# Kernel optimization log

Hardware: AMD Instinct MI355X
Metric: run time of the kernel (lower is better)

The kernel has to match this reference:

```python
import jax, jax.numpy as jnp
import numpy as np

B, S, FEAT, HID, H = 8, 1024, 1024, 1024, 8
DH = HID // H  # head dim = 128
MASK_VAL = -128.0  # mask_val = -2**7 (soft additive mask, per original code)


def setup_inputs() -> dict:
    key = jax.random.key(0)
    ks = jax.random.split(key, 4)
    scale = 0.02
    return {
        "queries": jax.random.normal(ks[0], (B, S, FEAT), dtype=jnp.float32),
        "Wq": jax.random.normal(ks[1], (FEAT, HID), dtype=jnp.float32) * scale,
        "bq": jnp.zeros((HID,), dtype=jnp.float32),
        "Wk": jax.random.normal(ks[2], (FEAT, HID), dtype=jnp.float32) * scale,
        "bk": jnp.zeros((HID,), dtype=jnp.float32),
        "Wv": jax.random.normal(ks[3], (FEAT, HID), dtype=jnp.float32) * scale,
        "bv": jnp.zeros((HID,), dtype=jnp.float32),
    }


def reference(queries, Wq, bq, Wk, bk, Wv, bv):
    # Self-attention: keys = values = queries (torch forward defaults)
    q = queries @ Wq + bq  # [B,S,HID]
    k = queries @ Wk + bk
    v = queries @ Wv + bv
    # split heads: chunk along last dim == reshape (B,S,H,DH)
    qh = q.reshape(B, S, H, DH)
    kh = k.reshape(B, S, H, DH)
    vh = v.reshape(B, S, H, DH)
    # exp-scaled-dot score (non-standard: exp BEFORE mask/softmax)
    logits = jnp.einsum("bqhd,bkhd->bhqk", qh, kh) / np.float32(np.sqrt(DH))
    score = jnp.exp(logits)
    # soft additive causal mask: upper triangle (diag=1) gets -128
    mask = jnp.triu(jnp.full((S, S), MASK_VAL, dtype=score.dtype), k=1)
    att = jax.nn.softmax(score + mask, axis=-1)  # [B,H,S,S]
    ctx = jnp.einsum("bhqk,bkhd->bqhd", att, vh)  # [B,S,H,DH]
    # reverse heads: concat along last dim
    return ctx.reshape(B, S, HID)
```

## Files before the change

### kernel.cpp

```cpp
#include <hip/hip_runtime.h>


typedef __bf16 bf16x8 __attribute__((ext_vector_type(8)));
typedef float floatx4 __attribute__((ext_vector_type(4)));
typedef unsigned short u16;
typedef unsigned int u32;

#define RSCALE 0.08838834764831845f

__device__ __forceinline__ u16 f2b(float f) {
  union { float f; unsigned u; } v; v.f = f;
  return (u16)((v.u + 0x7FFFu + ((v.u >> 16) & 1u)) >> 16);
}

__device__ __forceinline__ void gld_lds16(const void* g, void* l) {
  __builtin_amdgcn_global_load_lds(
      (const __attribute__((address_space(1))) unsigned*)g,
      (__attribute__((address_space(3))) unsigned*)l, 16, 0, 0);
}

#define MFMA16(a, b, c) __builtin_amdgcn_mfma_f32_16x16x32_bf16(a, b, c, 0, 0, 0)

__global__ __launch_bounds__(256) void prep_kernel(
    const float4* __restrict__ X, u16* __restrict__ Xb,
    const float* __restrict__ Wq, const float* __restrict__ Wk,
    const float* __restrict__ Wv, u16* __restrict__ Wtb) {
  if (blockIdx.x < 8192) {
    unsigned i = blockIdx.x * 256u + threadIdx.x;
    float4 v = X[i];
    ushort4 o;
    o.x = f2b(v.x); o.y = f2b(v.y); o.z = f2b(v.z); o.w = f2b(v.w);
    *reinterpret_cast<ushort4*>(Xb + 4u * i) = o;
  } else {
    const int bid = blockIdx.x - 8192;
    const int mat = bid >> 10;
    const int bx = bid & 31, by = (bid >> 5) & 31;
    const float* W = (mat == 0) ? Wq : (mat == 1) ? Wk : Wv;
    u16* Wt = Wtb + (size_t)mat * (1024u * 1024u);
    __shared__ u16 tile[32][33];
    const int x = threadIdx.x & 31, y = threadIdx.x >> 5;
    const int kt = bx * 32, nt = by * 32;
#pragma unroll
    for (int i = 0; i < 4; ++i)
      tile[y + 8 * i][x] = f2b(W[(size_t)(kt + y + 8 * i) * 1024 + nt + x]);
    __syncthreads();
#pragma unroll
    for (int i = 0; i < 4; ++i)
      Wt[(size_t)(nt + y + 8 * i) * 1024 + kt + x] = tile[x][y + 8 * i];
  }
}

__global__ __launch_bounds__(256, 2) void gemm_qkv_kernel(
    const u16* __restrict__ Xb, const u16* __restrict__ Wtb,
    const float* __restrict__ bq, const float* __restrict__ bk,
    const float* __restrict__ bv, u16* __restrict__ Qh, u16* __restrict__ Kh,
    u16* __restrict__ Vt) {
  const int mat = blockIdx.z;
  const u16* __restrict__ Wt = Wtb + (size_t)mat * (1024u * 1024u);
  const float* __restrict__ bias = (mat == 0) ? bq : (mat == 1) ? bk : bv;

  const int m0 = blockIdx.x * 128;
  const int n0 = blockIdx.y * 128;

  __shared__ u16 As[2][128 * 64];
  __shared__ u16 Bs[2][128 * 64];

  const int tid = threadIdx.x;
  const int wid = tid >> 6;
  const int lane = tid & 63;
  const int quad = lane >> 4;
  const int l16 = lane & 15;
  const int wm = (wid & 1) * 64;
  const int wn = (wid >> 1) * 64;

  const floatx4 z4 = {0.f, 0.f, 0.f, 0.f};
  floatx4 acc[4][4];
#pragma unroll
  for (int i = 0; i < 4; ++i)
#pragma unroll
    for (int j = 0; j < 4; ++j) acc[i][j] = z4;

  const int srow = wid * 32;
  const int lrow = lane >> 3;
  const int gblk = (lane & 7) ^ lrow;

  auto stage = [&](int b, int k0) {
#pragma unroll
    for (int c = 0; c < 4; ++c) {
      const int row = srow + c * 8 + lrow;
      gld_lds16(Xb + (size_t)(m0 + row) * 1024 + k0 + gblk * 8,
                As[b] + (srow + c * 8) * 64);
      gld_lds16(Wt + (size_t)(n0 + row) * 1024 + k0 + gblk * 8,
                Bs[b] + (srow + c * 8) * 64);
    }
  };

  stage(0, 0);

  for (int i = 0; i < 16; ++i) {
    __syncthreads();
    if (i < 15) stage((i + 1) & 1, (i + 1) * 64);

    const u16* __restrict__ Ab = As[i & 1];
    const u16* __restrict__ Bb = Bs[i & 1];
#pragma unroll
    for (int c = 0; c < 2; ++c) {
      const int phys = ((c * 4 + quad) ^ (l16 & 7)) * 8;
      bf16x8 af[4], bfr[4];
#pragma unroll
      for (int ii = 0; ii < 4; ++ii)
        af[ii] = *(const bf16x8*)(Ab + (wm + ii * 16 + l16) * 64 + phys);
#pragma unroll
      for (int j = 0; j < 4; ++j)
        bfr[j] = *(const bf16x8*)(Bb + (wn + j * 16 + l16) * 64 + phys);
#pragma unroll
      for (int ii = 0; ii < 4; ++ii)
#pragma unroll
        for (int j = 0; j < 4; ++j)
          acc[ii][j] = MFMA16(af[ii], bfr[j], acc[ii][j]);
    }
  }

  const int b = m0 >> 10;
  const int h = n0 >> 7;
  const int sbase = (m0 & 1023) + wm;
  float bv4[4];
#pragma unroll
  for (int j = 0; j < 4; ++j) bv4[j] = bias[n0 + wn + j * 16 + l16];

  if (mat < 2) {
    u16* outp = (mat == 0 ? Qh : Kh) + (size_t)(b * 8 + h) * 1024 * 128;
#pragma unroll
    for (int i = 0; i < 4; ++i)
#pragma unroll
      for (int j = 0; j < 4; ++j) {
        const int d = wn + j * 16 + l16;
#pragma unroll
        for (int r = 0; r < 4; ++r) {
          const int s = sbase + i * 16 + quad * 4 + r;
          outp[(size_t)s * 128 + d] = f2b(acc[i][j][r] + bv4[j]);
        }
      }
  } else {
    u16* outp = Vt + (size_t)(b * 8 + h) * 128 * 1024;
#pragma unroll
    for (int i = 0; i < 4; ++i)
#pragma unroll
      for (int j = 0; j < 4; ++j) {
        const int d = wn + j * 16 + l16;
        const int s = sbase + i * 16 + quad * 4;
        ushort4 pk;
        pk.x = f2b(acc[i][j][0] + bv4[j]);
        pk.y = f2b(acc[i][j][1] + bv4[j]);
        pk.z = f2b(acc[i][j][2] + bv4[j]);
        pk.w = f2b(acc[i][j][3] + bv4[j]);
        *(ushort4*)(outp + (size_t)d * 1024 + s) = pk;
      }
  }
}

__global__ __launch_bounds__(256, 2) void attn_kernel(const u16* __restrict__ Qh,
                                                      const u16* __restrict__ Kh,
                                                      const u16* __restrict__ Vt,
                                                      float* __restrict__ out) {
  const int id = blockIdx.x;
  const int x = id & 7;
  const int j = id >> 3;
  const int bh = x * 8 + (j & 7);
  const int QTMAP[8] = {7, 5, 6, 4, 0, 2, 1, 3};
  const int qt = QTMAP[j >> 3];
  const int q0 = qt * 128;

  const int tid = threadIdx.x;
  const int wid = tid >> 6;
  const int lane = tid & 63;
  const int quad = lane >> 4;
  const int l16 = lane & 15;

  __shared__ u16 Ks[2][64 * 128];
  __shared__ u16 Vs[2][128 * 64];
  __shared__ u16 Ps[4][32 * 32];

  const u16* __restrict__ Qbase = Qh + (size_t)bh * 1024 * 128;
  const u16* __restrict__ Kbase = Kh + (size_t)bh * 1024 * 128;
  const u16* __restrict__ Vbase = Vt + (size_t)bh * 128 * 1024;

  const int qw = q0 + wid * 32;

  bf16x8 qf[2][4];
#pragma unroll
  for (int nt = 0; nt < 2; ++nt)
#pragma unroll
    for (int c = 0; c < 4; ++c)
      qf[nt][c] = *(const bf16x8*)(Qbase + (size_t)(qw + nt * 16 + l16) * 128 +
                                   c * 32 + quad * 8);

  const floatx4 z4 = {0.f, 0.f, 0.f, 0.f};
  floatx4 o[2][8];
#pragma unroll
  for (int nt = 0; nt < 2; ++nt)
#pragma unroll
    for (int dt = 0; dt < 8; ++dt) o[nt][dt] = z4;
  float lacc[2] = {0.f, 0.f};

  auto stage = [&](int b, int k0) {
#pragma unroll
    for (int c = 0; c < 4; ++c) {
      const int r0 = wid * 16 + c * 4;
      const int row = r0 + quad;
      gld_lds16(Kbase + (size_t)(k0 + row) * 128 + ((l16 ^ (c * 4 + quad)) * 8),
                Ks[b] + r0 * 128);
    }
#pragma unroll
    for (int c = 0; c < 4; ++c) {
      const int r0 = wid * 32 + c * 8;
      const int row = r0 + (lane >> 3);
      gld_lds16(Vbase + (size_t)row * 1024 + k0 +
                    (((lane & 7) ^ ((lane >> 3) & 7)) * 8),
                Vs[b] + r0 * 64);
    }
  };

  const int n = (q0 + 128) >> 6;
  stage(0, 0);

  for (int i = 0; i < n; ++i) {
    const int k0 = i << 6;
    __syncthreads();
    if (i + 1 < n) stage((i + 1) & 1, k0 + 64);

    const u16* __restrict__ Kb = Ks[i & 1];
    const u16* __restrict__ Vb = Vs[i & 1];

#pragma unroll
    for (int half = 0; half < 2; ++half) {
      if (k0 + half * 32 > qw + 31) break;

#pragma unroll
      for (int f2 = 0; f2 < 2; ++f2) {
        const int f = half * 2 + f2;
        bf16x8 kf[4];
#pragma unroll
        for (int c = 0; c < 4; ++c)
          kf[c] = *(const bf16x8*)(Kb + (f * 16 + l16) * 128 +
                                   (((c * 4 + quad) ^ l16) * 8));
        floatx4 st[2];
#pragma unroll
        for (int nt = 0; nt < 2; ++nt) {
          st[nt] = z4;
#pragma unroll
          for (int c = 0; c < 4; ++c) st[nt] = MFMA16(kf[c], qf[nt][c], st[nt]);
        }
        const int kb = k0 + f * 16 + quad * 4;
#pragma unroll
        for (int nt = 0; nt < 2; ++nt) {
          const int qrow = qw + nt * 16 + l16;
          float p[4];
#pragma unroll
          for (int r = 0; r < 4; ++r) {
            const float e = fminf(__expf(st[nt][r] * RSCALE), 85.f);
            p[r] = (kb + r > qrow) ? 0.f : __expf(e);
          }
          lacc[nt] += (p[0] + p[1]) + (p[2] + p[3]);
          uint2 pk;
          pk.x = (u32)f2b(p[0]) | ((u32)f2b(p[1]) << 16);
          pk.y = (u32)f2b(p[2]) | ((u32)f2b(p[3]) << 16);
          *(uint2*)((char*)Ps[wid] + (nt * 16 + l16) * 64 +
                    (((f2 * 2 + (quad >> 1)) ^ (l16 & 3)) * 16) +
                    (quad & 1) * 8) = pk;
        }
      }
      asm volatile("s_waitcnt lgkmcnt(0)" ::: "memory");

      bf16x8 pa[2];
#pragma unroll
      for (int nt = 0; nt < 2; ++nt)
        pa[nt] = *(const bf16x8*)((char*)Ps[wid] + (nt * 16 + l16) * 64 +
                                  ((quad ^ (l16 & 3)) * 16));
#pragma unroll
      for (int dt = 0; dt < 8; ++dt) {
        const bf16x8 vf = *(const bf16x8*)(
            Vb + (dt * 16 + l16) * 64 +
            (((half * 4 + quad) ^ (l16 & 7)) * 8));
        o[0][dt] = MFMA16(vf, pa[0], o[0][dt]);
        o[1][dt] = MFMA16(vf, pa[1], o[1][dt]);
      }
    }
  }

  float linv[2];
#pragma unroll
  for (int nt = 0; nt < 2; ++nt) {
    float s = lacc[nt];
    s += __shfl_xor(s, 16);
    s += __shfl_xor(s, 32);
    linv[nt] = 1.0f / s;
  }

  float* outp = out + (size_t)(bh >> 3) * 1024 * 1024 + (bh & 7) * 128;
#pragma unroll
  for (int nt = 0; nt < 2; ++nt) {
    const int qrow = qw + nt * 16 + l16;
#pragma unroll
    for (int dt = 0; dt < 8; ++dt) {
      float4 v;
      v.x = o[nt][dt][0] * linv[nt];
      v.y = o[nt][dt][1] * linv[nt];
      v.z = o[nt][dt][2] * linv[nt];
      v.w = o[nt][dt][3] * linv[nt];
      *(float4*)(outp + (size_t)qrow * 1024 + dt * 16 + quad * 4) = v;
    }
  }
}

extern "C" void kernel_launch(void* const* d_in, const int* in_sizes, int n_in,
                              void* d_out, int out_size, void* d_ws,
                              size_t ws_size, hipStream_t stream) {
  const float* X = (const float*)d_in[0];
  const float* Wq = (const float*)d_in[1];
  const float* bq = (const float*)d_in[2];
  const float* Wk = (const float*)d_in[3];
  const float* bk = (const float*)d_in[4];
  const float* Wv = (const float*)d_in[5];
  const float* bv = (const float*)d_in[6];
  float* out = (float*)d_out;

  char* ws = (char*)d_ws;
  u16* Xb  = (u16*)(ws);
  u16* Wtb = (u16*)(ws + (16u << 20));
  u16* Qh  = (u16*)(ws + (22u << 20));
  u16* Kh  = (u16*)(ws + (38u << 20));
  u16* Vt  = (u16*)(ws + (54u << 20));

  prep_kernel<<<8192 + 3072, 256, 0, stream>>>((const float4*)X, Xb, Wq, Wk,
                                               Wv, Wtb);
  dim3 gg(64, 8, 3);
  gemm_qkv_kernel<<<gg, 256, 0, stream>>>(Xb, Wtb, bq, bk, bv, Qh, Kh, Vt);
  attn_kernel<<<512, 256, 0, stream>>>(Qh, Kh, Vt, out);
}
```

Baseline: 198.7 us.

## Split prep and QKV GEMM into separate launches, shrink attention key tile to 32

```diff
diff --git a/kernel.cpp b/kernel.cpp
--- a/kernel.cpp
+++ b/kernel.cpp
@@ -21,43 +21,37 @@
 
 #define MFMA16(a, b, c) __builtin_amdgcn_mfma_f32_16x16x32_bf16(a, b, c, 0, 0, 0)
 
-__global__ __launch_bounds__(256) void prep_kernel(
-    const float4* __restrict__ X, u16* __restrict__ Xb,
+__global__ __launch_bounds__(256) void cast_kernel(const float4* __restrict__ X,
+                                                   u16* __restrict__ Xb) {
+  unsigned i = blockIdx.x * 256u + threadIdx.x;
+  float4 v = X[i];
+  ushort4 o;
+  o.x = f2b(v.x); o.y = f2b(v.y); o.z = f2b(v.z); o.w = f2b(v.w);
+  *reinterpret_cast<ushort4*>(Xb + 4u * i) = o;
+}
+
+__global__ __launch_bounds__(256) void transpose_kernel(
     const float* __restrict__ Wq, const float* __restrict__ Wk,
     const float* __restrict__ Wv, u16* __restrict__ Wtb) {
-  if (blockIdx.x < 8192) {
-    unsigned i = blockIdx.x * 256u + threadIdx.x;
-    float4 v = X[i];
-    ushort4 o;
-    o.x = f2b(v.x); o.y = f2b(v.y); o.z = f2b(v.z); o.w = f2b(v.w);
-    *reinterpret_cast<ushort4*>(Xb + 4u * i) = o;
-  } else {
-    const int bid = blockIdx.x - 8192;
-    const int mat = bid >> 10;
-    const int bx = bid & 31, by = (bid >> 5) & 31;
-    const float* W = (mat == 0) ? Wq : (mat == 1) ? Wk : Wv;
-    u16* Wt = Wtb + (size_t)mat * (1024u * 1024u);
-    __shared__ u16 tile[32][33];
-    const int x = threadIdx.x & 31, y = threadIdx.x >> 5;
-    const int kt = bx * 32, nt = by * 32;
-#pragma unroll
-    for (int i = 0; i < 4; ++i)
-      tile[y + 8 * i][x] = f2b(W[(size_t)(kt + y + 8 * i) * 1024 + nt + x]);
-    __syncthreads();
-#pragma unroll
-    for (int i = 0; i < 4; ++i)
-      Wt[(size_t)(nt + y + 8 * i) * 1024 + kt + x] = tile[x][y + 8 * i];
-  }
+  const float* W = (blockIdx.z == 0) ? Wq : (blockIdx.z == 1) ? Wk : Wv;
+  u16* Wt = Wtb + (size_t)blockIdx.z * (1024u * 1024u);
+  __shared__ u16 tile[32][33];
+  const int x = threadIdx.x, y = threadIdx.y;
+  const int kt = blockIdx.x * 32, nt = blockIdx.y * 32;
+#pragma unroll
+  for (int i = 0; i < 4; ++i)
+    tile[y + 8 * i][x] = f2b(W[(size_t)(kt + y + 8 * i) * 1024 + nt + x]);
+  __syncthreads();
+#pragma unroll
+  for (int i = 0; i < 4; ++i)
+    Wt[(size_t)(nt + y + 8 * i) * 1024 + kt + x] = tile[x][y + 8 * i];
 }
 
 __global__ __launch_bounds__(256, 2) void gemm_qkv_kernel(
     const u16* __restrict__ Xb, const u16* __restrict__ Wtb,
-    const float* __restrict__ bq, const float* __restrict__ bk,
-    const float* __restrict__ bv, u16* __restrict__ Qh, u16* __restrict__ Kh,
-    u16* __restrict__ Vt) {
-  const int mat = blockIdx.z;
+    const float* __restrict__ bias, u16* __restrict__ outQK,
+    u16* __restrict__ outVt, const int mat) {
   const u16* __restrict__ Wt = Wtb + (size_t)mat * (1024u * 1024u);
-  const float* __restrict__ bias = (mat == 0) ? bq : (mat == 1) ? bk : bv;
 
   const int m0 = blockIdx.x * 128;
   const int n0 = blockIdx.y * 128;
@@ -129,7 +123,7 @@
   for (int j = 0; j < 4; ++j) bv4[j] = bias[n0 + wn + j * 16 + l16];
 
   if (mat < 2) {
-    u16* outp = (mat == 0 ? Qh : Kh) + (size_t)(b * 8 + h) * 1024 * 128;
+    u16* outp = outQK + (size_t)(b * 8 + h) * 1024 * 128;
 #pragma unroll
     for (int i = 0; i < 4; ++i)
 #pragma unroll
@@ -142,7 +136,7 @@
         }
       }
   } else {
-    u16* outp = Vt + (size_t)(b * 8 + h) * 128 * 1024;
+    u16* outp = outVt + (size_t)(b * 8 + h) * 128 * 1024;
 #pragma unroll
     for (int i = 0; i < 4; ++i)
 #pragma unroll
@@ -164,11 +158,9 @@
                                                       const u16* __restrict__ Vt,
                                                       float* __restrict__ out) {
   const int id = blockIdx.x;
-  const int x = id & 7;
-  const int j = id >> 3;
-  const int bh = x * 8 + (j & 7);
-  const int QTMAP[8] = {7, 5, 6, 4, 0, 2, 1, 3};
-  const int qt = QTMAP[j >> 3];
+  const int bh = (id & 7) * 8 + ((id >> 3) & 7);
+  const int QTMAP[8] = {7, 4, 6, 5, 0, 3, 1, 2};
+  const int qt = QTMAP[id >> 6];
   const int q0 = qt * 128;
 
   const int tid = threadIdx.x;
@@ -177,9 +169,9 @@
   const int quad = lane >> 4;
   const int l16 = lane & 15;
 
-  __shared__ u16 Ks[2][64 * 128];
-  __shared__ u16 Vs[2][128 * 64];
-  __shared__ u16 Ps[4][32 * 32];
+  __shared__ u16 Ks[2][32 * 128];
+  __shared__ u16 Vs[2][64 * 64];
+  __shared__ u16 Ps[4][16 * 64];
 
   const u16* __restrict__ Qbase = Qh + (size_t)bh * 1024 * 128;
   const u16* __restrict__ Kbase = Kh + (size_t)bh * 1024 * 128;
@@ -203,42 +195,41 @@
     for (int dt = 0; dt < 8; ++dt) o[nt][dt] = z4;
   float lacc[2] = {0.f, 0.f};
 
+  const int slr = lane >> 3;
+  const int sp = lane & 7;
+  const int ssub = sp >> 2;
+
   auto stage = [&](int b, int k0) {
 #pragma unroll
-    for (int c = 0; c < 4; ++c) {
-      const int r0 = wid * 16 + c * 4;
+    for (int c = 0; c < 2; ++c) {
+      const int r0 = wid * 8 + c * 4;
       const int row = r0 + quad;
-      gld_lds16(Kbase + (size_t)(k0 + row) * 128 + ((l16 ^ (c * 4 + quad)) * 8),
+      gld_lds16(Kbase + (size_t)(k0 + row) * 128 + ((l16 ^ (row & 15)) * 8),
                 Ks[b] + r0 * 128);
     }
 #pragma unroll
-    for (int c = 0; c < 4; ++c) {
-      const int r0 = wid * 32 + c * 8;
-      const int row = r0 + (lane >> 3);
-      gld_lds16(Vbase + (size_t)row * 1024 + k0 +
-                    (((lane & 7) ^ ((lane >> 3) & 7)) * 8),
-                Vs[b] + r0 * 64);
+    for (int c = 0; c < 2; ++c) {
+      const int r = wid * 16 + c * 8 + slr;
+      const int jj = (sp & 3) ^ (r & 3);
+      gld_lds16(Vbase + (size_t)(2 * r + ssub) * 1024 + k0 + jj * 8,
+                Vs[b] + (wid * 16 + c * 8) * 64);
     }
   };
 
-  const int n = (q0 + 128) >> 6;
+  const int n = (q0 + 128) >> 5;
   stage(0, 0);
 
   for (int i = 0; i < n; ++i) {
-    const int k0 = i << 6;
+    const int k0 = i << 5;
     __syncthreads();
-    if (i + 1 < n) stage((i + 1) & 1, k0 + 64);
-
-    const u16* __restrict__ Kb = Ks[i & 1];
-    const u16* __restrict__ Vb = Vs[i & 1];
-
-#pragma unroll
-    for (int half = 0; half < 2; ++half) {
-      if (k0 + half * 32 > qw + 31) break;
-
-#pragma unroll
-      for (int f2 = 0; f2 < 2; ++f2) {
-        const int f = half * 2 + f2;
+    if (i + 1 < n) stage((i + 1) & 1, k0 + 32);
+
+    if (k0 <= qw + 31) {
+      const u16* __restrict__ Kb = Ks[i & 1];
+      const u16* __restrict__ Vb = Vs[i & 1];
+
+#pragma unroll
+      for (int f = 0; f < 2; ++f) {
         bf16x8 kf[4];
 #pragma unroll
         for (int c = 0; c < 4; ++c)
@@ -265,23 +256,27 @@
           uint2 pk;
           pk.x = (u32)f2b(p[0]) | ((u32)f2b(p[1]) << 16);
           pk.y = (u32)f2b(p[2]) | ((u32)f2b(p[3]) << 16);
-          *(uint2*)((char*)Ps[wid] + (nt * 16 + l16) * 64 +
-                    (((f2 * 2 + (quad >> 1)) ^ (l16 & 3)) * 16) +
-                    (quad & 1) * 8) = pk;
+          const int prow = nt * 8 + (l16 >> 1);
+          const int s8 = f * 4 + quad;
+          *(uint2*)((char*)Ps[wid] + prow * 128 + (l16 & 1) * 64 +
+                    (((s8 >> 1) ^ (prow & 3)) * 16) + (s8 & 1) * 8) = pk;
         }
       }
       asm volatile("s_waitcnt lgkmcnt(0)" ::: "memory");
 
       bf16x8 pa[2];
 #pragma unroll
-      for (int nt = 0; nt < 2; ++nt)
-        pa[nt] = *(const bf16x8*)((char*)Ps[wid] + (nt * 16 + l16) * 64 +
-                                  ((quad ^ (l16 & 3)) * 16));
+      for (int nt = 0; nt < 2; ++nt) {
+        const int prow = nt * 8 + (l16 >> 1);
+        pa[nt] = *(const bf16x8*)((char*)Ps[wid] + prow * 128 +
+                                  (l16 & 1) * 64 + ((quad ^ (prow & 3)) * 16));
+      }
 #pragma unroll
       for (int dt = 0; dt < 8; ++dt) {
-        const bf16x8 vf = *(const bf16x8*)(
-            Vb + (dt * 16 + l16) * 64 +
-            (((half * 4 + quad) ^ (l16 & 7)) * 8));
+        const int d = dt * 16 + l16;
+        const int vr = d >> 1;
+        const bf16x8 vf = *(const bf16x8*)(Vb + vr * 64 + (d & 1) * 32 +
+                                           ((quad ^ (vr & 3)) * 8));
         o[0][dt] = MFMA16(vf, pa[0], o[0][dt]);
         o[1][dt] = MFMA16(vf, pa[1], o[1][dt]);
       }
@@ -332,9 +327,12 @@
   u16* Kh  = (u16*)(ws + (38u << 20));
   u16* Vt  = (u16*)(ws + (54u << 20));
 
-  prep_kernel<<<8192 + 3072, 256, 0, stream>>>((const float4*)X, Xb, Wq, Wk,
-                                               Wv, Wtb);
-  dim3 gg(64, 8, 3);
-  gemm_qkv_kernel<<<gg, 256, 0, stream>>>(Xb, Wtb, bq, bk, bv, Qh, Kh, Vt);
+  cast_kernel<<<8192, 256, 0, stream>>>((const float4*)X, Xb);
+  dim3 gt(32, 32, 3), bt(32, 8);
+  transpose_kernel<<<gt, bt, 0, stream>>>(Wq, Wk, Wv, Wtb);
+  dim3 gg(64, 8);
+  gemm_qkv_kernel<<<gg, 256, 0, stream>>>(Xb, Wtb, bq, Qh, Vt, 0);
+  gemm_qkv_kernel<<<gg, 256, 0, stream>>>(Xb, Wtb, bk, Kh, Vt, 1);
+  gemm_qkv_kernel<<<gg, 256, 0, stream>>>(Xb, Wtb, bv, Qh, Vt, 2);
   attn_kernel<<<512, 256, 0, stream>>>(Qh, Kh, Vt, out);
 }
```

After: 213.0 us. 1.07x slower.
